# Kernel tuning notes

Hardware: AMD Instinct MI355X
Metric: run time of the kernel (lower is better)

Reference implementation:

```python
import jax, jax.numpy as jnp
import numpy as np

N = 50000   # nodes
E = 800000  # edges (avg degree 16)
C = 128     # hidden_channels
G = 128     # graphs in batch
L0, L1 = 512, 256  # linear_hidden_channels
P = 2       # num_params (output per graph)


def setup_inputs() -> dict:
    key = jax.random.key(0)
    ks = iter(jax.random.split(key, 48))

    def w(shape):
        return jax.random.normal(next(ks), shape, jnp.float32) / np.float32(np.sqrt(shape[0]))

    inp = {}
    inp["x"] = jax.random.normal(next(ks), (N, 4), jnp.float32)
    inp["edge_index"] = jax.random.randint(next(ks), (2, E), 0, N, dtype=jnp.int32)
    inp["edge_attr"] = jax.random.normal(next(ks), (E, 3), jnp.float32)
    inp["batch"] = jnp.sort(jax.random.randint(next(ks), (N,), 0, G, dtype=jnp.int32))
    # TransformerConv params: layer 0 (in=4) and shared layer (in=C, applied twice
    # because `[GConv(...)]*(n-1)` reuses the same module object).
    for i, din in enumerate([4, C]):
        inp[f"Wq{i}"] = w((din, C)); inp[f"bq{i}"] = jnp.zeros((C,), jnp.float32)
        inp[f"Wk{i}"] = w((din, C)); inp[f"bk{i}"] = jnp.zeros((C,), jnp.float32)
        inp[f"Wv{i}"] = w((din, C)); inp[f"bv{i}"] = jnp.zeros((C,), jnp.float32)
        inp[f"We{i}"] = w((3, C))   # lin_edge has no bias
        inp[f"Ws{i}"] = w((din, C)); inp[f"bs{i}"] = jnp.zeros((C,), jnp.float32)
    inp["Wl0"] = w((C, L0));  inp["bl0"] = jnp.zeros((L0,), jnp.float32)
    inp["Wl1"] = w((L0, L1)); inp["bl1"] = jnp.zeros((L1,), jnp.float32)
    inp["Wl2"] = w((L1, P));  inp["bl2"] = jnp.zeros((P,), jnp.float32)
    return inp


def tconv(x, src, dst, e_attr, Wq, bq, Wk, bk, Wv, bv, We, Ws, bs):
    # TransformerConv (heads=1, edge_dim, root_weight=True, beta=False)
    n = x.shape[0]
    c = Wq.shape[1]
    q = x @ Wq + bq            # [N, C]
    k = x @ Wk + bk
    v = x @ Wv + bv
    e = e_attr @ We            # [E, C]
    kj = k[src] + e            # [E, C] key at source + edge emb
    vj = v[src] + e            # [E, C] value at source + edge emb
    logits = jnp.sum(q[dst] * kj, axis=-1) / jnp.sqrt(jnp.float32(c))  # [E]
    # softmax over incoming edges of each target node
    m = jax.ops.segment_max(logits, dst, num_segments=n)
    a = jnp.exp(logits - m[dst])
    denom = jax.ops.segment_sum(a, dst, num_segments=n)
    alpha = a / denom[dst]
    out = jax.ops.segment_sum(vj * alpha[:, None], dst, num_segments=n)
    return out + x @ Ws + bs   # root/skip connection


def reference(x, edge_index, edge_attr, batch,
              Wq0, bq0, Wk0, bk0, Wv0, bv0, We0, Ws0, bs0,
              Wq1, bq1, Wk1, bk1, Wv1, bv1, We1, Ws1, bs1,
              Wl0, bl0, Wl1, bl1, Wl2, bl2):
    src, dst = edge_index[0], edge_index[1]
    # layer 0
    h = tconv(x, src, dst, edge_attr, Wq0, bq0, Wk0, bk0, Wv0, bv0, We0, Ws0, bs0)
    h = jax.nn.leaky_relu(h, 0.01)  # dropout is identity in eval
    # layers 1..2 share weights (Python list-multiplication of modules)
    for _ in range(2):
        h = tconv(h, src, dst, edge_attr, Wq1, bq1, Wk1, bk1, Wv1, bv1, We1, Ws1, bs1)
        h = jax.nn.leaky_relu(h, 0.01)
    # global_add_pool
    g = jax.ops.segment_sum(h, batch, num_segments=G)  # [G, C]
    # MLP head
    g = jax.nn.relu(g @ Wl0 + bl0)
    g = jax.nn.relu(g @ Wl1 + bl1)
    g = g @ Wl2 + bl2                                  # [G, 2]
    return jnp.ravel(g)                                # [G*2]
```

## Files before the change

kernel.cpp:

```cpp
#include <hip/hip_runtime.h>
#include <math.h>

#define N_NODES 50000
#define N_EDGES 800000
#define CDIM    128
#define GDIM    128
#define L0DIM   512
#define L1DIM   256

typedef unsigned int uint;
typedef unsigned short ushort;
typedef __attribute__((ext_vector_type(8))) short short8;
typedef __attribute__((ext_vector_type(4))) float f32x4;

#define QSCALE 0.12751744f

__device__ inline ushort f2bf(float f) {
  uint u = __float_as_uint(f);
  uint r = (u + 0x7fffu + ((u >> 16) & 1u)) >> 16;
  return (ushort)r;
}
__device__ inline float bflo(uint u) { return __uint_as_float(u << 16); }
__device__ inline float bfhi(uint u) { return __uint_as_float(u & 0xffff0000u); }
__device__ inline uint pack2bf(float a, float b) {
  return (uint)f2bf(a) | ((uint)f2bf(b) << 16);
}

__global__ void hist_kernel(const int* __restrict__ dst, int* counts, int E) {
  int e = blockIdx.x * 256 + threadIdx.x;
  if (e < E) atomicAdd(&counts[dst[e]], 1);
}

__global__ void scan_blocks(const int* __restrict__ counts, int* excl, int* bsums, int N) {
  __shared__ int s[1024];
  int tid = threadIdx.x;
  int i = blockIdx.x * 1024 + tid;
  int v = (i < N) ? counts[i] : 0;
  s[tid] = v;
  __syncthreads();
  for (int off = 1; off < 1024; off <<= 1) {
    int t = (tid >= off) ? s[tid - off] : 0;
    __syncthreads();
    s[tid] += t;
    __syncthreads();
  }
  if (i < N) excl[i] = s[tid] - v;
  if (tid == 1023) bsums[blockIdx.x] = s[1023];
}

__global__ void scan_sums(int* bsums, int nb) {
  int lane = threadIdx.x;
  int orig = (lane < nb) ? bsums[lane] : 0;
  int v = orig;
#pragma unroll
  for (int off = 1; off < 64; off <<= 1) {
    int t = __shfl_up(v, off);
    if (lane >= off) v += t;
  }
  if (lane < nb) bsums[lane] = v - orig;
}

__global__ void scan_add(const int* __restrict__ excl, const int* __restrict__ bsums,
                         int* indptr, int N, int E) {
  int i = blockIdx.x * 1024 + threadIdx.x;
  if (i < N) indptr[i] = excl[i] + bsums[blockIdx.x];
  if (i == 0) indptr[N] = E;
}

__global__ void scatter2_kernel(const int* __restrict__ dst, const int* __restrict__ src,
                                const float* __restrict__ attr,
                                const int* __restrict__ indptr,
                                int* cursor, int* csr_src, float4* csr_attr, int E) {
  int e = blockIdx.x * 256 + threadIdx.x;
  if (e < E) {
    int d = dst[e];
    int pos = atomicAdd(&cursor[d], 1);
    int i = indptr[d] + pos;
    csr_src[i] = src[e];
    csr_attr[i] = make_float4(attr[e * 3 + 0], attr[e * 3 + 1], attr[e * 3 + 2], 0.f);
  }
}

__global__ void l0_qkvs(const float* __restrict__ x,
                        const float* __restrict__ Wq, const float* __restrict__ bq,
                        const float* __restrict__ Wk, const float* __restrict__ bk,
                        const float* __restrict__ Wv, const float* __restrict__ bv,
                        const float* __restrict__ Ws, const float* __restrict__ bs,
                        ushort* __restrict__ q, ushort* __restrict__ kvb,
                        float* __restrict__ hs, ushort* __restrict__ hb16, int N) {
  __shared__ float W[4][4][128];
  __shared__ float B[4][128];
  int tid = threadIdx.x;
  for (int i = tid; i < 4 * 128; i += 256) {
    W[0][i >> 7][i & 127] = Wq[i];
    W[1][i >> 7][i & 127] = Wk[i];
    W[2][i >> 7][i & 127] = Wv[i];
    W[3][i >> 7][i & 127] = Ws[i];
  }
  for (int i = tid; i < 128; i += 256) {
    B[0][i] = bq[i]; B[1][i] = bk[i]; B[2][i] = bv[i]; B[3][i] = bs[i];
  }
  __syncthreads();
  int gid = blockIdx.x * 256 + tid;
  int n = gid >> 7, c = gid & 127;
  if (n >= N) return;
  float x0 = x[n * 4 + 0], x1 = x[n * 4 + 1], x2 = x[n * 4 + 2], x3 = x[n * 4 + 3];
  float qv = x0 * W[0][0][c] + x1 * W[0][1][c] + x2 * W[0][2][c] + x3 * W[0][3][c] + B[0][c];
  float kv = x0 * W[1][0][c] + x1 * W[1][1][c] + x2 * W[1][2][c] + x3 * W[1][3][c] + B[1][c];
  float vv = x0 * W[2][0][c] + x1 * W[2][1][c] + x2 * W[2][2][c] + x3 * W[2][3][c] + B[2][c];
  float sv = x0 * W[3][0][c] + x1 * W[3][1][c] + x2 * W[3][2][c] + x3 * W[3][3][c] + B[3][c];
  q[(size_t)n * 128 + c] = f2bf(qv * QSCALE);
  kvb[(size_t)n * 256 + c]       = f2bf(kv);
  kvb[(size_t)n * 256 + 128 + c] = f2bf(vv);
  hs[(size_t)n * 128 + c] = sv;
  hb16[(size_t)n * 128 + c] = f2bf(sv);
}

__global__ void prep_w(const float* __restrict__ Wq, const float* __restrict__ Wk,
                       const float* __restrict__ Wv, const float* __restrict__ Ws,
                       ushort* __restrict__ wt) {
  int idx = blockIdx.x * 256 + threadIdx.x;
  int z = idx >> 14, rem = idx & 16383;
  int k_ = rem >> 7, c_ = rem & 127;
  const float* W = (z == 0) ? Wq : (z == 1) ? Wk : (z == 2) ? Wv : Ws;
  wt[z * 16384 + c_ * 128 + k_] = f2bf(W[k_ * 128 + c_]);
}

#define LDA 136
__global__ __launch_bounds__(256) void gemm_mfma(
    const ushort* __restrict__ H16, const ushort* __restrict__ wtg,
    const float* __restrict__ bq, const float* __restrict__ bk,
    const float* __restrict__ bv, const float* __restrict__ bs,
    ushort* __restrict__ q, ushort* __restrict__ kvb,
    float* __restrict__ hs, int N) {
  int z = blockIdx.z;
  const float* bb = (z == 0) ? bq : (z == 1) ? bk : (z == 2) ? bv : bs;
  __shared__ ushort Alds[64 * LDA];
  __shared__ ushort Wlds[128 * LDA];
  int tid = threadIdx.x;
  int n0 = blockIdx.x * 64;

  {
    const uint* wg = (const uint*)(wtg + z * 16384);
    uint* wl = (uint*)Wlds;
    for (int i = tid; i < 8192; i += 256) {
      int c_ = i >> 6, kp = i & 63;
      wl[c_ * (LDA / 2) + kp] = wg[c_ * 64 + kp];
    }
  }
  {
    const uint* hg = (const uint*)H16;
    uint* al = (uint*)Alds;
    for (int i = tid; i < 4096; i += 256) {
      int r = i >> 6, kp = i & 63;
      int grow = n0 + r; grow = (grow < N) ? grow : (N - 1);
      al[r * (LDA / 2) + kp] = hg[(size_t)grow * 64 + kp];
    }
  }
  __syncthreads();

  int w = tid >> 6, lane = tid & 63;
  int m_ = lane & 15, quad = lane >> 4;
  f32x4 acc[8];
#pragma unroll
  for (int ct = 0; ct < 8; ct++) acc[ct] = 0.f;

#pragma unroll
  for (int kc = 0; kc < 4; kc++) {
    short8 af = *(const short8*)&Alds[(w * 16 + m_) * LDA + kc * 32 + quad * 8];
#pragma unroll
    for (int ct = 0; ct < 8; ct++) {
      short8 bf = *(const short8*)&Wlds[(ct * 16 + m_) * LDA + kc * 32 + quad * 8];
      acc[ct] = __builtin_amdgcn_mfma_f32_16x16x32_bf16(af, bf, acc[ct], 0, 0, 0);
    }
  }

#pragma unroll
  for (int ct = 0; ct < 8; ct++) {
    int col = ct * 16 + m_;
    float bcol = bb[col];
#pragma unroll
    for (int reg = 0; reg < 4; reg++) {
      int n = n0 + w * 16 + quad * 4 + reg;
      if (n < N) {
        float o = acc[ct][reg] + bcol;
        if (z == 0)      q[(size_t)n * 128 + col] = f2bf(o * QSCALE);
        else if (z == 3) hs[(size_t)n * 128 + col] = o;
        else             kvb[(size_t)n * 256 + ((z == 2) ? 128 : 0) + col] = f2bf(o);
      }
    }
  }
}

__global__ __launch_bounds__(256) void attn_fused(
    const ushort* __restrict__ q, const ushort* __restrict__ kv,
    const int* __restrict__ indptr, const int* __restrict__ csr_src,
    const float4* __restrict__ csr_attr, const float* __restrict__ We,
    float* __restrict__ h, ushort* __restrict__ hb16, int N) {
  __shared__ float WeS[384];
  int tid = threadIdx.x;
  for (int i = tid; i < 384; i += 256) WeS[i] = We[i];
  __syncthreads();
  int lane = tid & 63;
  int n = blockIdx.x * 4 + (tid >> 6);
  if (n >= N) return;
  int g = lane >> 4, gl = lane & 15;
  int c = gl * 8;
  uint4 qr = *(const uint4*)&q[(size_t)n * 128 + c];
  float qv[8] = {bflo(qr.x), bfhi(qr.x), bflo(qr.y), bfhi(qr.y),
                 bflo(qr.z), bfhi(qr.z), bflo(qr.w), bfhi(qr.w)};
  float we0[8], we1[8], we2[8];
#pragma unroll
  for (int j = 0; j < 8; j++) {
    we0[j] = WeS[c + j]; we1[j] = WeS[128 + c + j]; we2[j] = WeS[256 + c + j];
  }
  float t0 = 0.f, t1 = 0.f, t2 = 0.f;
#pragma unroll
  for (int j = 0; j < 8; j++) {
    t0 = fmaf(we0[j], qv[j], t0);
    t1 = fmaf(we1[j], qv[j], t1);
    t2 = fmaf(we2[j], qv[j], t2);
  }
#pragma unroll
  for (int off = 1; off < 16; off <<= 1) {
    t0 += __shfl_xor(t0, off);
    t1 += __shfl_xor(t1, off);
    t2 += __shfl_xor(t2, off);
  }

  float4 sk0 = *(const float4*)&h[(size_t)n * 128 + c];
  float4 sk1 = *(const float4*)&h[(size_t)n * 128 + c + 4];
  int beg = indptr[n], end = indptr[n + 1];

  if (end > beg) {
    float d = 0.f;
    float sa0 = 0.f, sa1 = 0.f, sa2 = 0.f;
    float acc[8];
#pragma unroll
    for (int j = 0; j < 8; j++) acc[j] = 0.f;
    const uint* kvw = (const uint*)kv;
    const int endm1 = end - 1;

    int i = beg + g;
    int pA = (i     < end) ? i     : endm1;
    int pB = (i + 4 < end) ? i + 4 : endm1;
    int sjA = csr_src[pA];  float4 atA = csr_attr[pA];
    int sjB = csr_src[pB];  float4 atB = csr_attr[pB];

    for (; i < end; i += 8) {
      int sjAc = sjA, sjBc = sjB;
      float4 atAc = atA, atBc = atB;
      float wB = ((i + 4) < end) ? 1.f : 0.f;
      int nn = i + 8;
      int qA = (nn     < end) ? nn     : endm1;
      int qB = (nn + 4 < end) ? nn + 4 : endm1;
      sjA = csr_src[qA]; atA = csr_attr[qA];
      sjB = csr_src[qB]; atB = csr_attr[qB];
      const uint4* kpA = (const uint4*)(kvw + (size_t)sjAc * 128);
      const uint4* kpB = (const uint4*)(kvw + (size_t)sjBc * 128);
      uint4 krA = kpA[gl];
      uint4 krB = kpB[gl];
      uint4 vrA = kpA[16 + gl];
      uint4 vrB = kpB[16 + gl];
      float kxA[8], kxB[8];
      kxA[0] = bflo(krA.x); kxA[1] = bfhi(krA.x); kxA[2] = bflo(krA.y); kxA[3] = bfhi(krA.y);
      kxA[4] = bflo(krA.z); kxA[5] = bfhi(krA.z); kxA[6] = bflo(krA.w); kxA[7] = bfhi(krA.w);
      kxB[0] = bflo(krB.x); kxB[1] = bfhi(krB.x); kxB[2] = bflo(krB.y); kxB[3] = bfhi(krB.y);
      kxB[4] = bflo(krB.z); kxB[5] = bfhi(krB.z); kxB[6] = bflo(krB.w); kxB[7] = bfhi(krB.w);
      float pAv = 0.f, pBv = 0.f;
#pragma unroll
      for (int j = 0; j < 8; j++) {
        pAv = fmaf(qv[j], kxA[j], pAv);
        pBv = fmaf(qv[j], kxB[j], pBv);
      }
      pAv += __shfl_xor(pAv, 1);  pBv += __shfl_xor(pBv, 1);
      pAv += __shfl_xor(pAv, 2);  pBv += __shfl_xor(pBv, 2);
      pAv += __shfl_xor(pAv, 4);  pBv += __shfl_xor(pBv, 4);
      pAv += __shfl_xor(pAv, 8);  pBv += __shfl_xor(pBv, 8);
      pAv = fmaf(atAc.x, t0, pAv);
      pBv = fmaf(atBc.x, t0, pBv);
      pAv = fmaf(atAc.y, t1, pAv);
      pBv = fmaf(atBc.y, t1, pBv);
      pAv = fmaf(atAc.z, t2, pAv);
      pBv = fmaf(atBc.z, t2, pBv);
      float aA = __builtin_amdgcn_exp2f(pAv);
      float aB = wB * __builtin_amdgcn_exp2f(pBv);
      d += aA + aB;
      sa0 = fmaf(aA, atAc.x, sa0); sa0 = fmaf(aB, atBc.x, sa0);
      sa1 = fmaf(aA, atAc.y, sa1); sa1 = fmaf(aB, atBc.y, sa1);
      sa2 = fmaf(aA, atAc.z, sa2); sa2 = fmaf(aB, atBc.z, sa2);
      float vxA[8], vxB[8];
      vxA[0] = bflo(vrA.x); vxA[1] = bfhi(vrA.x); vxA[2] = bflo(vrA.y); vxA[3] = bfhi(vrA.y);
      vxA[4] = bflo(vrA.z); vxA[5] = bfhi(vrA.z); vxA[6] = bflo(vrA.w); vxA[7] = bfhi(vrA.w);
      vxB[0] = bflo(vrB.x); vxB[1] = bfhi(vrB.x); vxB[2] = bflo(vrB.y); vxB[3] = bfhi(vrB.y);
      vxB[4] = bflo(vrB.z); vxB[5] = bfhi(vrB.z); vxB[6] = bflo(vrB.w); vxB[7] = bfhi(vrB.w);
#pragma unroll
      for (int j = 0; j < 8; j++) {
        acc[j] = fmaf(aA, vxA[j], acc[j]);
        acc[j] = fmaf(aB, vxB[j], acc[j]);
      }
    }
#pragma unroll
    for (int off = 16; off < 64; off <<= 1) {
      d += __shfl_xor(d, off);
      sa0 += __shfl_xor(sa0, off);
      sa1 += __shfl_xor(sa1, off);
      sa2 += __shfl_xor(sa2, off);
#pragma unroll
      for (int j = 0; j < 8; j++) acc[j] += __shfl_xor(acc[j], off);
    }
    float inv = 1.f / d;
    float o[8];
#pragma unroll
    for (int j = 0; j < 8; j++) {
      float ecorr = sa0 * we0[j] + sa1 * we1[j] + sa2 * we2[j];
      o[j] = (acc[j] + ecorr) * inv;
    }
    sk0.x += o[0]; sk0.y += o[1]; sk0.z += o[2]; sk0.w += o[3];
    sk1.x += o[4]; sk1.y += o[5]; sk1.z += o[6]; sk1.w += o[7];
  }
  sk0.x = (sk0.x > 0.f) ? sk0.x : 0.01f * sk0.x;
  sk0.y = (sk0.y > 0.f) ? sk0.y : 0.01f * sk0.y;
  sk0.z = (sk0.z > 0.f) ? sk0.z : 0.01f * sk0.z;
  sk0.w = (sk0.w > 0.f) ? sk0.w : 0.01f * sk0.w;
  sk1.x = (sk1.x > 0.f) ? sk1.x : 0.01f * sk1.x;
  sk1.y = (sk1.y > 0.f) ? sk1.y : 0.01f * sk1.y;
  sk1.z = (sk1.z > 0.f) ? sk1.z : 0.01f * sk1.z;
  sk1.w = (sk1.w > 0.f) ? sk1.w : 0.01f * sk1.w;
  if (g == 0) {
    *(float4*)&h[(size_t)n * 128 + c] = sk0;
    *(float4*)&h[(size_t)n * 128 + c + 4] = sk1;
    uint4 hb;
    hb.x = pack2bf(sk0.x, sk0.y);
    hb.y = pack2bf(sk0.z, sk0.w);
    hb.z = pack2bf(sk1.x, sk1.y);
    hb.w = pack2bf(sk1.z, sk1.w);
    *(uint4*)&hb16[(size_t)n * 128 + c] = hb;
  }
}

__global__ void pool_kernel(const float* __restrict__ h, const int* __restrict__ batch,
                            float* __restrict__ gout, int N) {
  int tid = threadIdx.x;
  int sub = tid >> 6;
  int c = 2 * (tid & 63);
  int n0 = blockIdx.x * 64 + sub * 16;
  if (n0 >= N) return;
  int n1 = min(n0 + 16, N);
  float a0 = 0.f, a1 = 0.f;
  int cur = batch[n0];
  for (int n = n0; n < n1; n++) {
    int b = batch[n];
    if (b != cur) {
      atomicAdd(&gout[cur * 128 + c], a0);
      atomicAdd(&gout[cur * 128 + c + 1], a1);
      a0 = 0.f; a1 = 0.f; cur = b;
    }
    float2 hv = *(const float2*)&h[(size_t)n * 128 + c];
    a0 += hv.x; a1 += hv.y;
  }
  atomicAdd(&gout[cur * 128 + c], a0);
  atomicAdd(&gout[cur * 128 + c + 1], a1);
}

__global__ __launch_bounds__(256) void mlp_fused(
    const float* __restrict__ gp,
    const float* __restrict__ Wl0, const float* __restrict__ bl0,
    const float* __restrict__ Wl1, const float* __restrict__ bl1,
    const float* __restrict__ Wl2, const float* __restrict__ bl2,
    float* __restrict__ out) {
  int g = blockIdx.x;
  int tid = threadIdx.x;
  __shared__ float xin[CDIM];
  __shared__ float h1[L0DIM];
  __shared__ float h2[L1DIM];
  __shared__ float r0s[4], r1s[4];
  if (tid < CDIM) xin[tid] = gp[g * CDIM + tid];
  __syncthreads();
  for (int c = tid; c < L0DIM; c += 256) {
    float a0 = 0.f, a1 = 0.f, a2 = 0.f, a3 = 0.f;
#pragma unroll 4
    for (int kk = 0; kk < CDIM; kk += 4) {
      a0 = fmaf(xin[kk + 0], Wl0[(kk + 0) * L0DIM + c], a0);
      a1 = fmaf(xin[kk + 1], Wl0[(kk + 1) * L0DIM + c], a1);
      a2 = fmaf(xin[kk + 2], Wl0[(kk + 2) * L0DIM + c], a2);
      a3 = fmaf(xin[kk + 3], Wl0[(kk + 3) * L0DIM + c], a3);
    }
    h1[c] = fmaxf((a0 + a1) + (a2 + a3) + bl0[c], 0.f);
  }
  __syncthreads();
  {
    int c = tid;
    float a0 = 0.f, a1 = 0.f, a2 = 0.f, a3 = 0.f;
#pragma unroll 4
    for (int kk = 0; kk < L0DIM; kk += 4) {
      a0 = fmaf(h1[kk + 0], Wl1[(kk + 0) * L1DIM + c], a0);
      a1 = fmaf(h1[kk + 1], Wl1[(kk + 1) * L1DIM + c], a1);
      a2 = fmaf(h1[kk + 2], Wl1[(kk + 2) * L1DIM + c], a2);
      a3 = fmaf(h1[kk + 3], Wl1[(kk + 3) * L1DIM + c], a3);
    }
    h2[c] = fmaxf((a0 + a1) + (a2 + a3) + bl1[c], 0.f);
  }
  __syncthreads();
  float p0 = h2[tid] * Wl2[tid * 2 + 0];
  float p1 = h2[tid] * Wl2[tid * 2 + 1];
#pragma unroll
  for (int off = 32; off > 0; off >>= 1) {
    p0 += __shfl_down(p0, off);
    p1 += __shfl_down(p1, off);
  }
  int wv = tid >> 6, ln = tid & 63;
  if (ln == 0) { r0s[wv] = p0; r1s[wv] = p1; }
  __syncthreads();
  if (tid == 0) out[g * 2 + 0] = r0s[0] + r0s[1] + r0s[2] + r0s[3] + bl2[0];
  if (tid == 1) out[g * 2 + 1] = r1s[0] + r1s[1] + r1s[2] + r1s[3] + bl2[1];
}

extern "C" void kernel_launch(void* const* d_in, const int* in_sizes, int n_in,
                              void* d_out, int out_size, void* d_ws, size_t ws_size,
                              hipStream_t stream) {
  const int N = N_NODES, E = N_EDGES;
  const float* x    = (const float*)d_in[0];
  const int*   ei   = (const int*)d_in[1];
  const float* attr = (const float*)d_in[2];
  const int*   batch= (const int*)d_in[3];
  const int* src = ei;
  const int* dst = ei + E;

  const float *Wq0 = (const float*)d_in[4],  *bq0 = (const float*)d_in[5];
  const float *Wk0 = (const float*)d_in[6],  *bk0 = (const float*)d_in[7];
  const float *Wv0 = (const float*)d_in[8],  *bv0 = (const float*)d_in[9];
  const float *We0 = (const float*)d_in[10];
  const float *Ws0 = (const float*)d_in[11], *bs0 = (const float*)d_in[12];
  const float *Wq1 = (const float*)d_in[13], *bq1 = (const float*)d_in[14];
  const float *Wk1 = (const float*)d_in[15], *bk1 = (const float*)d_in[16];
  const float *Wv1 = (const float*)d_in[17], *bv1 = (const float*)d_in[18];
  const float *We1 = (const float*)d_in[19];
  const float *Ws1 = (const float*)d_in[20], *bs1 = (const float*)d_in[21];
  const float *Wl0 = (const float*)d_in[22], *bl0 = (const float*)d_in[23];
  const float *Wl1 = (const float*)d_in[24], *bl1 = (const float*)d_in[25];
  const float *Wl2 = (const float*)d_in[26], *bl2 = (const float*)d_in[27];

  size_t off = 0;
  auto carve = [&](size_t bytes) {
    void* p = (char*)d_ws + off;
    off += (bytes + 255) & ~(size_t)255;
    return p;
  };
  float*  hA       = (float*)carve((size_t)N * CDIM * 4);
  float*  hB       = (float*)carve((size_t)N * CDIM * 4);
  ushort* hA16     = (ushort*)carve((size_t)N * CDIM * 2);
  ushort* hB16     = (ushort*)carve((size_t)N * CDIM * 2);
  ushort* qb       = (ushort*)carve((size_t)N * CDIM * 2);
  ushort* kvb      = (ushort*)carve((size_t)N * 256 * 2);
  int*    indptr   = (int*)carve((size_t)(N + 1) * 4);
  int*    csr_src  = (int*)carve((size_t)E * 4);
  float4* csr_attr = (float4*)carve((size_t)E * 16);
  int*    cc       = (int*)carve((size_t)2 * N * 4);
  int*    counts   = cc;
  int*    cursor   = cc + N;
  int*    excl     = (int*)carve((size_t)N * 4);
  int*    bsums    = (int*)carve((size_t)64 * 4);
  ushort* wt1      = (ushort*)carve((size_t)4 * 16384 * 2);
  float*  gp       = (float*)carve((size_t)GDIM * CDIM * 4);

  hipMemsetAsync(cc, 0, (size_t)2 * N * 4, stream);
  hipMemsetAsync(gp, 0, (size_t)GDIM * CDIM * 4, stream);

  int nscan = (N + 1023) / 1024;
  hist_kernel<<<(E + 255) / 256, 256, 0, stream>>>(dst, counts, E);
  scan_blocks<<<nscan, 1024, 0, stream>>>(counts, excl, bsums, N);
  scan_sums<<<1, 64, 0, stream>>>(bsums, nscan);
  scan_add<<<nscan, 1024, 0, stream>>>(excl, bsums, indptr, N, E);
  scatter2_kernel<<<(E + 255) / 256, 256, 0, stream>>>(dst, src, attr, indptr, cursor,
                                                       csr_src, csr_attr, E);
  prep_w<<<256, 256, 0, stream>>>(Wq1, Wk1, Wv1, Ws1, wt1);

  int naBlocks = (N + 3) / 4;
  dim3 gemmGrid((N + 63) / 64, 1, 4);

  l0_qkvs<<<(N * 128 + 255) / 256, 256, 0, stream>>>(
      x, Wq0, bq0, Wk0, bk0, Wv0, bv0, Ws0, bs0, qb, kvb, hA, hA16, N);
  attn_fused<<<naBlocks, 256, 0, stream>>>(qb, kvb, indptr, csr_src, csr_attr, We0,
                                           hA, hA16, N);

  gemm_mfma<<<gemmGrid, 256, 0, stream>>>(hA16, wt1, bq1, bk1, bv1, bs1, qb, kvb, hB, N);
  attn_fused<<<naBlocks, 256, 0, stream>>>(qb, kvb, indptr, csr_src, csr_attr, We1,
                                           hB, hB16, N);

  gemm_mfma<<<gemmGrid, 256, 0, stream>>>(hB16, wt1, bq1, bk1, bv1, bs1, qb, kvb, hA, N);
  attn_fused<<<naBlocks, 256, 0, stream>>>(qb, kvb, indptr, csr_src, csr_attr, We1,
                                           hA, hA16, N);

  pool_kernel<<<(N + 63) / 64, 256, 0, stream>>>(hA, batch, gp, N);
  mlp_fused<<<GDIM, 256, 0, stream>>>(gp, Wl0, bl0, Wl1, bl1, Wl2, bl2, (float*)d_out);
}
```

Baseline: 580.6 us.

## Pack source index into edge attr float4 and drop fp32 hidden-state writes

Stores the source node index in the unused w lane of the CSR edge-attribute float4, so the attention loop fetches one 16-byte record per edge instead of an int plus a float4. Attention no longer writes the fp32 hidden state and writes only a bf16 copy. Pooling now reads that bf16 output, and the cursor zeroing moves into scan_add to shrink the memset. This cuts global traffic per layer, but the pooled features are now summed from bf16-rounded values, which adds rounding error.

```diff
diff --git a/kernel.cpp b/kernel.cpp
--- a/kernel.cpp
+++ b/kernel.cpp
@@ -61,23 +61,27 @@
 }
 
 __global__ void scan_add(const int* __restrict__ excl, const int* __restrict__ bsums,
-                         int* indptr, int N, int E) {
+                         int* indptr, int* cursor, int N, int E) {
   int i = blockIdx.x * 1024 + threadIdx.x;
-  if (i < N) indptr[i] = excl[i] + bsums[blockIdx.x];
+  if (i < N) { indptr[i] = excl[i] + bsums[blockIdx.x]; cursor[i] = 0; }
   if (i == 0) indptr[N] = E;
 }
 
 __global__ void scatter2_kernel(const int* __restrict__ dst, const int* __restrict__ src,
                                 const float* __restrict__ attr,
                                 const int* __restrict__ indptr,
-                                int* cursor, int* csr_src, float4* csr_attr, int E) {
+                                int* cursor, float4* csr_sa, int E) {
   int e = blockIdx.x * 256 + threadIdx.x;
   if (e < E) {
     int d = dst[e];
     int pos = atomicAdd(&cursor[d], 1);
     int i = indptr[d] + pos;
-    csr_src[i] = src[e];
-    csr_attr[i] = make_float4(attr[e * 3 + 0], attr[e * 3 + 1], attr[e * 3 + 2], 0.f);
+    float4 v;
+    v.x = attr[e * 3 + 0];
+    v.y = attr[e * 3 + 1];
+    v.z = attr[e * 3 + 2];
+    v.w = __int_as_float(src[e]);
+    csr_sa[i] = v;
   }
 }
 
@@ -87,7 +91,7 @@
                         const float* __restrict__ Wv, const float* __restrict__ bv,
                         const float* __restrict__ Ws, const float* __restrict__ bs,
                         ushort* __restrict__ q, ushort* __restrict__ kvb,
-                        float* __restrict__ hs, ushort* __restrict__ hb16, int N) {
+                        float* __restrict__ hs, int N) {
   __shared__ float W[4][4][128];
   __shared__ float B[4][128];
   int tid = threadIdx.x;
@@ -113,7 +117,6 @@
   kvb[(size_t)n * 256 + c]       = f2bf(kv);
   kvb[(size_t)n * 256 + 128 + c] = f2bf(vv);
   hs[(size_t)n * 128 + c] = sv;
-  hb16[(size_t)n * 128 + c] = f2bf(sv);
 }
 
 __global__ void prep_w(const float* __restrict__ Wq, const float* __restrict__ Wk,
@@ -194,9 +197,9 @@
 
 __global__ __launch_bounds__(256) void attn_fused(
     const ushort* __restrict__ q, const ushort* __restrict__ kv,
-    const int* __restrict__ indptr, const int* __restrict__ csr_src,
-    const float4* __restrict__ csr_attr, const float* __restrict__ We,
-    float* __restrict__ h, ushort* __restrict__ hb16, int N) {
+    const int* __restrict__ indptr, const float4* __restrict__ csr_sa,
+    const float* __restrict__ We,
+    const float* __restrict__ hskip, ushort* __restrict__ hout, int N) {
   __shared__ float WeS[384];
   int tid = threadIdx.x;
   for (int i = tid; i < 384; i += 256) WeS[i] = We[i];
@@ -228,8 +231,8 @@
     t2 += __shfl_xor(t2, off);
   }
 
-  float4 sk0 = *(const float4*)&h[(size_t)n * 128 + c];
-  float4 sk1 = *(const float4*)&h[(size_t)n * 128 + c + 4];
+  float4 sk0 = *(const float4*)&hskip[(size_t)n * 128 + c];
+  float4 sk1 = *(const float4*)&hskip[(size_t)n * 128 + c + 4];
   int beg = indptr[n], end = indptr[n + 1];
 
   if (end > beg) {
@@ -244,18 +247,19 @@
     int i = beg + g;
     int pA = (i     < end) ? i     : endm1;
     int pB = (i + 4 < end) ? i + 4 : endm1;
-    int sjA = csr_src[pA];  float4 atA = csr_attr[pA];
-    int sjB = csr_src[pB];  float4 atB = csr_attr[pB];
+    float4 saA = csr_sa[pA];
+    float4 saB = csr_sa[pB];
 
     for (; i < end; i += 8) {
-      int sjAc = sjA, sjBc = sjB;
-      float4 atAc = atA, atBc = atB;
+      float4 saAc = saA, saBc = saB;
       float wB = ((i + 4) < end) ? 1.f : 0.f;
       int nn = i + 8;
       int qA = (nn     < end) ? nn     : endm1;
       int qB = (nn + 4 < end) ? nn + 4 : endm1;
-      sjA = csr_src[qA]; atA = csr_attr[qA];
-      sjB = csr_src[qB]; atB = csr_attr[qB];
+      saA = csr_sa[qA];
+      saB = csr_sa[qB];
+      int sjAc = __float_as_int(saAc.w);
+      int sjBc = __float_as_int(saBc.w);
       const uint4* kpA = (const uint4*)(kvw + (size_t)sjAc * 128);
       const uint4* kpB = (const uint4*)(kvw + (size_t)sjBc * 128);
       uint4 krA = kpA[gl];
@@ -277,18 +281,18 @@
       pAv += __shfl_xor(pAv, 2);  pBv += __shfl_xor(pBv, 2);
       pAv += __shfl_xor(pAv, 4);  pBv += __shfl_xor(pBv, 4);
       pAv += __shfl_xor(pAv, 8);  pBv += __shfl_xor(pBv, 8);
-      pAv = fmaf(atAc.x, t0, pAv);
-      pBv = fmaf(atBc.x, t0, pBv);
-      pAv = fmaf(atAc.y, t1, pAv);
-      pBv = fmaf(atBc.y, t1, pBv);
-      pAv = fmaf(atAc.z, t2, pAv);
-      pBv = fmaf(atBc.z, t2, pBv);
+      pAv = fmaf(saAc.x, t0, pAv);
+      pBv = fmaf(saBc.x, t0, pBv);
+      pAv = fmaf(saAc.y, t1, pAv);
+      pBv = fmaf(saBc.y, t1, pBv);
+      pAv = fmaf(saAc.z, t2, pAv);
+      pBv = fmaf(saBc.z, t2, pBv);
       float aA = __builtin_amdgcn_exp2f(pAv);
       float aB = wB * __builtin_amdgcn_exp2f(pBv);
       d += aA + aB;
-      sa0 = fmaf(aA, atAc.x, sa0); sa0 = fmaf(aB, atBc.x, sa0);
-      sa1 = fmaf(aA, atAc.y, sa1); sa1 = fmaf(aB, atBc.y, sa1);
-      sa2 = fmaf(aA, atAc.z, sa2); sa2 = fmaf(aB, atBc.z, sa2);
+      sa0 = fmaf(aA, saAc.x, sa0); sa0 = fmaf(aB, saBc.x, sa0);
+      sa1 = fmaf(aA, saAc.y, sa1); sa1 = fmaf(aB, saBc.y, sa1);
+      sa2 = fmaf(aA, saAc.z, sa2); sa2 = fmaf(aB, saBc.z, sa2);
       float vxA[8], vxB[8];
       vxA[0] = bflo(vrA.x); vxA[1] = bfhi(vrA.x); vxA[2] = bflo(vrA.y); vxA[3] = bfhi(vrA.y);
       vxA[4] = bflo(vrA.z); vxA[5] = bfhi(vrA.z); vxA[6] = bflo(vrA.w); vxA[7] = bfhi(vrA.w);
@@ -328,18 +332,16 @@
   sk1.z = (sk1.z > 0.f) ? sk1.z : 0.01f * sk1.z;
   sk1.w = (sk1.w > 0.f) ? sk1.w : 0.01f * sk1.w;
   if (g == 0) {
-    *(float4*)&h[(size_t)n * 128 + c] = sk0;
-    *(float4*)&h[(size_t)n * 128 + c + 4] = sk1;
     uint4 hb;
     hb.x = pack2bf(sk0.x, sk0.y);
     hb.y = pack2bf(sk0.z, sk0.w);
     hb.z = pack2bf(sk1.x, sk1.y);
     hb.w = pack2bf(sk1.z, sk1.w);
-    *(uint4*)&hb16[(size_t)n * 128 + c] = hb;
-  }
-}
-
-__global__ void pool_kernel(const float* __restrict__ h, const int* __restrict__ batch,
+    *(uint4*)&hout[(size_t)n * 128 + c] = hb;
+  }
+}
+
+__global__ void pool_kernel(const ushort* __restrict__ h16, const int* __restrict__ batch,
                             float* __restrict__ gout, int N) {
   int tid = threadIdx.x;
   int sub = tid >> 6;
@@ -356,8 +358,8 @@
       atomicAdd(&gout[cur * 128 + c + 1], a1);
       a0 = 0.f; a1 = 0.f; cur = b;
     }
-    float2 hv = *(const float2*)&h[(size_t)n * 128 + c];
-    a0 += hv.x; a1 += hv.y;
+    uint hv = *(const uint*)&h16[(size_t)n * 128 + c];
+    a0 += bflo(hv); a1 += bfhi(hv);
   }
   atomicAdd(&gout[cur * 128 + c], a0);
   atomicAdd(&gout[cur * 128 + c + 1], a1);
@@ -454,8 +456,7 @@
   ushort* qb       = (ushort*)carve((size_t)N * CDIM * 2);
   ushort* kvb      = (ushort*)carve((size_t)N * 256 * 2);
   int*    indptr   = (int*)carve((size_t)(N + 1) * 4);
-  int*    csr_src  = (int*)carve((size_t)E * 4);
-  float4* csr_attr = (float4*)carve((size_t)E * 16);
+  float4* csr_sa   = (float4*)carve((size_t)E * 16);
   int*    cc       = (int*)carve((size_t)2 * N * 4);
   int*    counts   = cc;
   int*    cursor   = cc + N;
@@ -464,34 +465,31 @@
   ushort* wt1      = (ushort*)carve((size_t)4 * 16384 * 2);
   float*  gp       = (float*)carve((size_t)GDIM * CDIM * 4);
 
-  hipMemsetAsync(cc, 0, (size_t)2 * N * 4, stream);
+  hipMemsetAsync(counts, 0, (size_t)N * 4, stream);
   hipMemsetAsync(gp, 0, (size_t)GDIM * CDIM * 4, stream);
 
   int nscan = (N + 1023) / 1024;
   hist_kernel<<<(E + 255) / 256, 256, 0, stream>>>(dst, counts, E);
   scan_blocks<<<nscan, 1024, 0, stream>>>(counts, excl, bsums, N);
   scan_sums<<<1, 64, 0, stream>>>(bsums, nscan);
-  scan_add<<<nscan, 1024, 0, stream>>>(excl, bsums, indptr, N, E);
+  scan_add<<<nscan, 1024, 0, stream>>>(excl, bsums, indptr, cursor, N, E);
   scatter2_kernel<<<(E + 255) / 256, 256, 0, stream>>>(dst, src, attr, indptr, cursor,
-                                                       csr_src, csr_attr, E);
+                                                       csr_sa, E);
   prep_w<<<256, 256, 0, stream>>>(Wq1, Wk1, Wv1, Ws1, wt1);
 
   int naBlocks = (N + 3) / 4;
   dim3 gemmGrid((N + 63) / 64, 1, 4);
 
   l0_qkvs<<<(N * 128 + 255) / 256, 256, 0, stream>>>(
-      x, Wq0, bq0, Wk0, bk0, Wv0, bv0, Ws0, bs0, qb, kvb, hA, hA16, N);
-  attn_fused<<<naBlocks, 256, 0, stream>>>(qb, kvb, indptr, csr_src, csr_attr, We0,
-                                           hA, hA16, N);
+      x, Wq0, bq0, Wk0, bk0, Wv0, bv0, Ws0, bs0, qb, kvb, hA, N);
+  attn_fused<<<naBlocks, 256, 0, stream>>>(qb, kvb, indptr, csr_sa, We0, hA, hA16, N);
 
   gemm_mfma<<<gemmGrid, 256, 0, stream>>>(hA16, wt1, bq1, bk1, bv1, bs1, qb, kvb, hB, N);
-  attn_fused<<<naBlocks, 256, 0, stream>>>(qb, kvb, indptr, csr_src, csr_attr, We1,
-                                           hB, hB16, N);
+  attn_fused<<<naBlocks, 256, 0, stream>>>(qb, kvb, indptr, csr_sa, We1, hB, hB16, N);
 
   gemm_mfma<<<gemmGrid, 256, 0, stream>>>(hB16, wt1, bq1, bk1, bv1, bs1, qb, kvb, hA, N);
-  attn_fused<<<naBlocks, 256, 0, stream>>>(qb, kvb, indptr, csr_src, csr_attr, We1,
-                                           hA, hA16, N);
-
-  pool_kernel<<<(N + 63) / 64, 256, 0, stream>>>(hA, batch, gp, N);
+  attn_fused<<<naBlocks, 256, 0, stream>>>(qb, kvb, indptr, csr_sa, We1, hA, hA16, N);
+
+  pool_kernel<<<(N + 63) / 64, 256, 0, stream>>>(hA16, batch, gp, N);
   mlp_fused<<<GDIM, 256, 0, stream>>>(gp, Wl0, bl0, Wl1, bl1, Wl2, bl2, (float*)d_out);
 }
```

Result: faster. 566.1 us (-2.5%).
